# Optimization experiments

Measured on AMD Instinct MI355X. Metric: run time of the kernel, lower is better.

Reference implementation:

```python
import jax, jax.numpy as jnp
import numpy as np
import math

B, H, S, D = 2, 16, 2048, 64

def setup_inputs() -> dict:
    key = jax.random.key(0)
    kq, kk, kv, km = jax.random.split(key, 4)
    return {
        "query": jax.random.normal(kq, (B, H, S, D), dtype=jnp.float32),
        "key": jax.random.normal(kk, (B, H, S, D), dtype=jnp.float32),
        "value": jax.random.normal(kv, (B, H, S, D), dtype=jnp.float32),
        "attn_mask": jax.random.normal(km, (B, 1, S, S), dtype=jnp.float32),
    }

def reference(query, key, value, attn_mask):
    # qk = Q K^T / sqrt(D)  -> [B,H,S,S]
    scale = 1.0 / math.sqrt(query.shape[-1])
    qk = jnp.einsum("bhqd,bhkd->bhqk", query, key) * scale
    qk = qk + attn_mask  # additive mask, broadcasts over heads
    attn_weight = jax.nn.softmax(qk, axis=-1)
    # dropout_p = 0.0 (undefined global in source; p=0 train-mode dropout is identity)
    output = jnp.einsum("bhqk,bhkd->bhqd", attn_weight, value)
    return output
```

## Files before the change

### kernel.cpp

```cpp
#include <hip/hip_runtime.h>

#define B_ 2
#define H_ 16
#define S_ 2048
#define D_ 64

typedef __attribute__((ext_vector_type(8))) _Float16 half8;
typedef __attribute__((ext_vector_type(2))) __fp16 fp16x2;
typedef __attribute__((ext_vector_type(16))) float f32x16;

constexpr int QW  = 32;
constexpr int NW  = 2;
constexpr int QB  = QW * NW;
constexpr int KVB = 32;
constexpr int NIT = S_ / KVB;

__global__ __launch_bounds__(128, 2)
void fattn(const float* __restrict__ Qg, const float* __restrict__ Kg,
           const float* __restrict__ Vg, const float* __restrict__ Mg,
           float* __restrict__ Og)
{
    const int tid  = threadIdx.x;
    const int lo32 = tid & 31;
    const int hi   = (tid >> 5) & 1;
    const int wv   = tid >> 6;

    const int qblk = blockIdx.x;
    const int bh   = blockIdx.y;
    const int b    = bh >> 4;

    const float* Qp = Qg + (size_t)bh * S_ * D_;
    const float* Kp = Kg + (size_t)bh * S_ * D_;
    const float* Vp = Vg + (size_t)bh * S_ * D_;
    const float* Mp = Mg + (size_t)b  * S_ * S_;
    float*       Op = Og + (size_t)bh * S_ * D_;

    __shared__ __align__(16) _Float16 Khi[2][KVB * D_];
    __shared__ __align__(16) _Float16 Klo[2][KVB * D_];
    __shared__ __align__(16) _Float16 VThi[2][D_ * KVB];
    __shared__ __align__(16) _Float16 VTlo[2][D_ * KVB];

    const int qloc = qblk * QB + wv * QW + lo32;

    const int ksr = tid >> 2;
    const int ksc = tid & 3;
    const int vd  = tid & 63;
    const int vw  = tid >> 6;

    half8 Qhi[4], Qlo[4];
    #pragma unroll
    for (int f = 0; f < 4; ++f) {
        const float* src = Qp + (size_t)qloc * D_ + f * 16 + hi * 8;
        float4 a = *(const float4*)src;
        float4 c = *(const float4*)(src + 4);
        float v8[8] = {a.x, a.y, a.z, a.w, c.x, c.y, c.z, c.w};
        half8 hh, hl;
        #pragma unroll
        for (int j = 0; j < 8; ++j) {
            _Float16 h = (_Float16)v8[j];
            hh[j] = h;
            hl[j] = (_Float16)(v8[j] - (float)h);
        }
        Qhi[f] = hh; Qlo[f] = hl;
    }

    f32x16 acc0, acc1;
    #pragma unroll
    for (int i = 0; i < 16; ++i) { acc0[i] = 0.f; acc1[i] = 0.f; }
    float mrun = -1e30f, lrun = 0.f;

    const float kScL2 = 0.125f * 1.44269504088896340736f;
    const float kL2E  = 1.44269504088896340736f;

    float4 kr[4];
    float  vr[16];
    float4 mcur[4], mnxt[4];

    auto stage_load = [&](int kv) {
        const float* ks = Kp + (size_t)(kv + ksr) * D_ + ksc * 16;
        #pragma unroll
        for (int i = 0; i < 4; ++i) kr[i] = *(const float4*)(ks + 4 * i);
        const float* vs = Vp + (size_t)(kv + vw * 16) * D_ + vd;
        #pragma unroll
        for (int r = 0; r < 16; ++r) vr[r] = vs[(size_t)r * D_];
    };
    auto stage_write = [&](int bf) {
        #pragma unroll
        for (int u = 0; u < 2; ++u) {
            float e[8] = {kr[2*u].x, kr[2*u].y, kr[2*u].z, kr[2*u].w,
                          kr[2*u+1].x, kr[2*u+1].y, kr[2*u+1].z, kr[2*u+1].w};
            half8 hh, hl;
            #pragma unroll
            for (int j = 0; j < 8; ++j) {
                _Float16 h = (_Float16)e[j];
                hh[j] = h;
                hl[j] = (_Float16)(e[j] - (float)h);
            }
            const int cs = (ksc * 2 + u) ^ (ksr & 7);
            *(half8*)&Khi[bf][ksr * 64 + cs * 8] = hh;
            *(half8*)&Klo[bf][ksr * 64 + cs * 8] = hl;
        }
        #pragma unroll
        for (int u = 0; u < 2; ++u) {
            half8 hh, hl;
            #pragma unroll
            for (int j = 0; j < 8; ++j) {
                float x = vr[8*u + j];
                _Float16 h = (_Float16)x;
                hh[j] = h;
                hl[j] = (_Float16)(x - (float)h);
            }
            const int c = (vw * 2 + u) ^ (vd & 3) ^ ((vd >> 2) & 3);
            *(half8*)&VThi[bf][vd * 32 + c * 8] = hh;
            *(half8*)&VTlo[bf][vd * 32 + c * 8] = hl;
        }
    };
    auto mask_load = [&](int kv, float4* mv) {
        const float* mrow = Mp + (size_t)qloc * S_ + kv;
        #pragma unroll
        for (int g = 0; g < 4; ++g) mv[g] = *(const float4*)(mrow + 8 * g + 4 * hi);
    };

    stage_load(0);
    stage_write(0);
    mask_load(0, mcur);
    __syncthreads();

    for (int t = 0; t < NIT; ++t) {
        const int bf = t & 1;
        if (t + 1 < NIT) {
            mask_load((t + 1) * KVB, mnxt);
            stage_load((t + 1) * KVB);
        }

        f32x16 s;
        #pragma unroll
        for (int i = 0; i < 16; ++i) s[i] = 0.f;
        #pragma unroll
        for (int f = 0; f < 4; ++f) {
            const int cs = (2 * f + hi) ^ (lo32 & 7);
            half8 ah = *(const half8*)&Khi[bf][lo32 * 64 + cs * 8];
            half8 al = *(const half8*)&Klo[bf][lo32 * 64 + cs * 8];
            s = __builtin_amdgcn_mfma_f32_32x32x16_f16(ah, Qhi[f], s, 0, 0, 0);
            s = __builtin_amdgcn_mfma_f32_32x32x16_f16(al, Qhi[f], s, 0, 0, 0);
            s = __builtin_amdgcn_mfma_f32_32x32x16_f16(ah, Qlo[f], s, 0, 0, 0);
        }

        float p[16];
        #pragma unroll
        for (int g = 0; g < 4; ++g) {
            p[4*g+0] = fmaf(s[4*g+0], kScL2, mcur[g].x * kL2E);
            p[4*g+1] = fmaf(s[4*g+1], kScL2, mcur[g].y * kL2E);
            p[4*g+2] = fmaf(s[4*g+2], kScL2, mcur[g].z * kL2E);
            p[4*g+3] = fmaf(s[4*g+3], kScL2, mcur[g].w * kL2E);
        }

        float mt = p[0];
        #pragma unroll
        for (int r = 1; r < 16; ++r) mt = fmaxf(mt, p[r]);
        mt = fmaxf(mt, __shfl_xor(mt, 32));
        const float mnew = fmaxf(mrun, mt);
        const float corr = __builtin_amdgcn_exp2f(mrun - mnew);
        float ps = 0.f;
        #pragma unroll
        for (int r = 0; r < 16; ++r) {
            p[r] = __builtin_amdgcn_exp2f(p[r] - mnew);
            ps += p[r];
        }
        ps += __shfl_xor(ps, 32);
        lrun = lrun * corr + ps;
        mrun = mnew;
        #pragma unroll
        for (int i = 0; i < 16; ++i) { acc0[i] *= corr; acc1[i] *= corr; }

        int dw[8], px[8];
        #pragma unroll
        for (int g = 0; g < 4; ++g) {
            union { fp16x2 h; int i; } u0, u1;
            u0.h = __builtin_amdgcn_cvt_pkrtz(p[4*g+0], p[4*g+1]);
            u1.h = __builtin_amdgcn_cvt_pkrtz(p[4*g+2], p[4*g+3]);
            dw[2*g]   = u0.i;
            dw[2*g+1] = u1.i;
        }
        #pragma unroll
        for (int i = 0; i < 8; ++i) px[i] = __shfl_xor(dw[i], 32);

        half8 Pf[2];
        #pragma unroll
        for (int ks = 0; ks < 2; ++ks) {
            union { int i[4]; half8 h; } f;
            f.i[0] = hi ? px[4*ks+2] : dw[4*ks+0];
            f.i[1] = hi ? px[4*ks+3] : dw[4*ks+1];
            f.i[2] = hi ? dw[4*ks+2] : px[4*ks+0];
            f.i[3] = hi ? dw[4*ks+3] : px[4*ks+1];
            Pf[ks] = f.h;
        }

        #pragma unroll
        for (int ks = 0; ks < 2; ++ks) {
            const int c0 = (2 * ks + hi) ^ (lo32 & 3) ^ ((lo32 >> 2) & 3);
            half8 vh0 = *(const half8*)&VThi[bf][lo32        * 32 + c0 * 8];
            half8 vl0 = *(const half8*)&VTlo[bf][lo32        * 32 + c0 * 8];
            half8 vh1 = *(const half8*)&VThi[bf][(32 + lo32) * 32 + c0 * 8];
            half8 vl1 = *(const half8*)&VTlo[bf][(32 + lo32) * 32 + c0 * 8];
            acc0 = __builtin_amdgcn_mfma_f32_32x32x16_f16(vh0, Pf[ks], acc0, 0, 0, 0);
            acc0 = __builtin_amdgcn_mfma_f32_32x32x16_f16(vl0, Pf[ks], acc0, 0, 0, 0);
            acc1 = __builtin_amdgcn_mfma_f32_32x32x16_f16(vh1, Pf[ks], acc1, 0, 0, 0);
            acc1 = __builtin_amdgcn_mfma_f32_32x32x16_f16(vl1, Pf[ks], acc1, 0, 0, 0);
        }

        if (t + 1 < NIT) stage_write(bf ^ 1);
        #pragma unroll
        for (int g = 0; g < 4; ++g) mcur[g] = mnxt[g];
        __syncthreads();
    }

    const float inv = 1.0f / lrun;
    #pragma unroll
    for (int r = 0; r < 16; ++r) {
        const int drow = (r & 3) + 8 * (r >> 2) + 4 * hi;
        Op[(size_t)qloc * D_ + drow]      = acc0[r] * inv;
        Op[(size_t)qloc * D_ + 32 + drow] = acc1[r] * inv;
    }
}

extern "C" void kernel_launch(void* const* d_in, const int* in_sizes, int n_in,
                              void* d_out, int out_size, void* d_ws, size_t ws_size,
                              hipStream_t stream)
{
    (void)in_sizes; (void)n_in; (void)out_size; (void)d_ws; (void)ws_size;
    const float* Q = (const float*)d_in[0];
    const float* K = (const float*)d_in[1];
    const float* V = (const float*)d_in[2];
    const float* M = (const float*)d_in[3];
    float* O = (float*)d_out;

    dim3 grid(S_ / QB, B_ * H_);
    fattn<<<grid, 128, 0, stream>>>(Q, K, V, M, O);
}
```

Measured before the change: 241.0 us.

## Presplit K/V into fp16 hi/lo workspace and stream tiles via direct global-to-LDS loads

Adds a pre-pass kernel that converts K and V once into swizzled fp16 hi/lo tiles in the workspace. The attention kernel then copies each tile straight into LDS with global_load_lds, so each of the 32 query blocks per head no longer redoes the conversion and transpose work. It also adds a lazy rescale that skips the accumulator correction unless the running max grows by more than 8 (in log2 units). The cost is an extra kernel launch and a workspace round-trip, and it falls back to the old kernel if the workspace is too small.

```diff
diff --git a/kernel.cpp b/kernel.cpp
--- a/kernel.cpp
+++ b/kernel.cpp
@@ -14,6 +14,224 @@
 constexpr int QB  = QW * NW;
 constexpr int KVB = 32;
 constexpr int NIT = S_ / KVB;
+
+#define GLOBAL_AS(p) ((const __attribute__((address_space(1))) void*)(p))
+#define LDS_AS(p)    ((__attribute__((address_space(3))) void*)(p))
+
+__global__ __launch_bounds__(256)
+void presplit(const float* __restrict__ Kg, const float* __restrict__ Vg,
+              _Float16* __restrict__ W)
+{
+    const int t   = blockIdx.x;
+    const int bh  = blockIdx.y;
+    const int tid = threadIdx.x;
+
+    const float* Kp = Kg + (size_t)bh * S_ * D_ + (size_t)t * KVB * D_;
+    const float* Vp = Vg + (size_t)bh * S_ * D_ + (size_t)t * KVB * D_;
+    _Float16*    Wp = W + ((size_t)bh * NIT + t) * 8192;
+
+    {
+        const int r = tid >> 3, l = tid & 7;
+        const float* src = Kp + r * D_ + l * 8;
+        float4 a = *(const float4*)src;
+        float4 c = *(const float4*)(src + 4);
+        float e[8] = {a.x, a.y, a.z, a.w, c.x, c.y, c.z, c.w};
+        half8 hh, hl;
+        #pragma unroll
+        for (int j = 0; j < 8; ++j) {
+            _Float16 h = (_Float16)e[j];
+            hh[j] = h;
+            hl[j] = (_Float16)(e[j] - (float)h);
+        }
+        const int cs = l ^ (r & 7);
+        *(half8*)&Wp[r * 64 + cs * 8]        = hh;
+        *(half8*)&Wp[2048 + r * 64 + cs * 8] = hl;
+    }
+    {
+        const int d = tid & 63, c = tid >> 6;
+        float e[8];
+        #pragma unroll
+        for (int j = 0; j < 8; ++j) e[j] = Vp[(size_t)(c * 8 + j) * D_ + d];
+        half8 hh, hl;
+        #pragma unroll
+        for (int j = 0; j < 8; ++j) {
+            _Float16 h = (_Float16)e[j];
+            hh[j] = h;
+            hl[j] = (_Float16)(e[j] - (float)h);
+        }
+        const int cw = c ^ (d & 3) ^ ((d >> 2) & 3);
+        *(half8*)&Wp[4096 + d * 32 + cw * 8] = hh;
+        *(half8*)&Wp[6144 + d * 32 + cw * 8] = hl;
+    }
+}
+
+__global__ __launch_bounds__(128, 2)
+void fattn2(const float* __restrict__ Qg, const float* __restrict__ Mg,
+            const _Float16* __restrict__ W, float* __restrict__ Og)
+{
+    const int tid  = threadIdx.x;
+    const int lane = tid & 63;
+    const int lo32 = tid & 31;
+    const int hi   = (tid >> 5) & 1;
+    const int wv   = tid >> 6;
+
+    const int qblk = blockIdx.x;
+    const int bh   = blockIdx.y;
+    const int b    = bh >> 4;
+
+    const float* Qp = Qg + (size_t)bh * S_ * D_;
+    const float* Mp = Mg + (size_t)b  * S_ * S_;
+    float*       Op = Og + (size_t)bh * S_ * D_;
+    const _Float16* Wp = W + (size_t)bh * NIT * 8192;
+
+    __shared__ __align__(16) _Float16 TILE[2][8192];
+
+    const int qloc = qblk * QB + wv * QW + lo32;
+
+    half8 Qhi[4], Qlo[4];
+    #pragma unroll
+    for (int f = 0; f < 4; ++f) {
+        const float* src = Qp + (size_t)qloc * D_ + f * 16 + hi * 8;
+        float4 a = *(const float4*)src;
+        float4 c = *(const float4*)(src + 4);
+        float v8[8] = {a.x, a.y, a.z, a.w, c.x, c.y, c.z, c.w};
+        half8 hh, hl;
+        #pragma unroll
+        for (int j = 0; j < 8; ++j) {
+            _Float16 h = (_Float16)v8[j];
+            hh[j] = h;
+            hl[j] = (_Float16)(v8[j] - (float)h);
+        }
+        Qhi[f] = hh; Qlo[f] = hl;
+    }
+
+    f32x16 acc0, acc1;
+    #pragma unroll
+    for (int i = 0; i < 16; ++i) { acc0[i] = 0.f; acc1[i] = 0.f; }
+    float mrun = -1e30f, lrun = 0.f;
+
+    const float kScL2 = 0.125f * 1.44269504088896340736f;
+    const float kL2E  = 1.44269504088896340736f;
+
+    float4 mcur[4], mnxt[4];
+
+    auto stage = [&](int bf, int t) {
+        const _Float16* src = Wp + (size_t)t * 8192 + wv * 4096 + lane * 8;
+        _Float16* dst = &TILE[bf][wv * 4096];
+        #pragma unroll
+        for (int c = 0; c < 8; ++c)
+            __builtin_amdgcn_global_load_lds(GLOBAL_AS(src + c * 512),
+                                             LDS_AS(dst + c * 512), 16, 0, 0);
+    };
+    auto mask_load = [&](int kv, float4* mv) {
+        const float* mrow = Mp + (size_t)qloc * S_ + kv;
+        #pragma unroll
+        for (int g = 0; g < 4; ++g) mv[g] = *(const float4*)(mrow + 8 * g + 4 * hi);
+    };
+
+    stage(0, 0);
+    mask_load(0, mcur);
+    __syncthreads();
+
+    for (int t = 0; t < NIT; ++t) {
+        const int bf = t & 1;
+        if (t + 1 < NIT) {
+            mask_load((t + 1) * KVB, mnxt);
+            stage(bf ^ 1, t + 1);
+        }
+
+        f32x16 s;
+        #pragma unroll
+        for (int i = 0; i < 16; ++i) s[i] = 0.f;
+        #pragma unroll
+        for (int f = 0; f < 4; ++f) {
+            const int cs = (2 * f + hi) ^ (lo32 & 7);
+            half8 ah = *(const half8*)&TILE[bf][lo32 * 64 + cs * 8];
+            half8 al = *(const half8*)&TILE[bf][2048 + lo32 * 64 + cs * 8];
+            s = __builtin_amdgcn_mfma_f32_32x32x16_f16(ah, Qhi[f], s, 0, 0, 0);
+            s = __builtin_amdgcn_mfma_f32_32x32x16_f16(al, Qhi[f], s, 0, 0, 0);
+            s = __builtin_amdgcn_mfma_f32_32x32x16_f16(ah, Qlo[f], s, 0, 0, 0);
+        }
+
+        float p[16];
+        #pragma unroll
+        for (int g = 0; g < 4; ++g) {
+            p[4*g+0] = fmaf(s[4*g+0], kScL2, mcur[g].x * kL2E);
+            p[4*g+1] = fmaf(s[4*g+1], kScL2, mcur[g].y * kL2E);
+            p[4*g+2] = fmaf(s[4*g+2], kScL2, mcur[g].z * kL2E);
+            p[4*g+3] = fmaf(s[4*g+3], kScL2, mcur[g].w * kL2E);
+        }
+
+        float mt = p[0];
+        #pragma unroll
+        for (int r = 1; r < 16; ++r) mt = fmaxf(mt, p[r]);
+        mt = fmaxf(mt, __shfl_xor(mt, 32));
+        if (!__all(mt - mrun <= 8.0f)) {
+            const float mnew = fmaxf(mrun, mt);
+            const float corr = __builtin_amdgcn_exp2f(mrun - mnew);
+            lrun *= corr;
+            #pragma unroll
+            for (int i = 0; i < 16; ++i) { acc0[i] *= corr; acc1[i] *= corr; }
+            mrun = mnew;
+        }
+        float ps = 0.f;
+        #pragma unroll
+        for (int r = 0; r < 16; ++r) {
+            p[r] = __builtin_amdgcn_exp2f(p[r] - mrun);
+            ps += p[r];
+        }
+        ps += __shfl_xor(ps, 32);
+        lrun += ps;
+
+        int dw[8], px[8];
+        #pragma unroll
+        for (int g = 0; g < 4; ++g) {
+            union { fp16x2 h; int i; } u0, u1;
+            u0.h = __builtin_amdgcn_cvt_pkrtz(p[4*g+0], p[4*g+1]);
+            u1.h = __builtin_amdgcn_cvt_pkrtz(p[4*g+2], p[4*g+3]);
+            dw[2*g]   = u0.i;
+            dw[2*g+1] = u1.i;
+        }
+        #pragma unroll
+        for (int i = 0; i < 8; ++i) px[i] = __shfl_xor(dw[i], 32);
+
+        half8 Pf[2];
+        #pragma unroll
+        for (int ks = 0; ks < 2; ++ks) {
+            union { int i[4]; half8 h; } f;
+            f.i[0] = hi ? px[4*ks+2] : dw[4*ks+0];
+            f.i[1] = hi ? px[4*ks+3] : dw[4*ks+1];
+            f.i[2] = hi ? dw[4*ks+2] : px[4*ks+0];
+            f.i[3] = hi ? dw[4*ks+3] : px[4*ks+1];
+            Pf[ks] = f.h;
+        }
+
+        #pragma unroll
+        for (int ks = 0; ks < 2; ++ks) {
+            const int c0 = (2 * ks + hi) ^ (lo32 & 3) ^ ((lo32 >> 2) & 3);
+            half8 vh0 = *(const half8*)&TILE[bf][4096 + lo32        * 32 + c0 * 8];
+            half8 vl0 = *(const half8*)&TILE[bf][6144 + lo32        * 32 + c0 * 8];
+            half8 vh1 = *(const half8*)&TILE[bf][4096 + (32 + lo32) * 32 + c0 * 8];
+            half8 vl1 = *(const half8*)&TILE[bf][6144 + (32 + lo32) * 32 + c0 * 8];
+            acc0 = __builtin_amdgcn_mfma_f32_32x32x16_f16(vh0, Pf[ks], acc0, 0, 0, 0);
+            acc0 = __builtin_amdgcn_mfma_f32_32x32x16_f16(vl0, Pf[ks], acc0, 0, 0, 0);
+            acc1 = __builtin_amdgcn_mfma_f32_32x32x16_f16(vh1, Pf[ks], acc1, 0, 0, 0);
+            acc1 = __builtin_amdgcn_mfma_f32_32x32x16_f16(vl1, Pf[ks], acc1, 0, 0, 0);
+        }
+
+        #pragma unroll
+        for (int g = 0; g < 4; ++g) mcur[g] = mnxt[g];
+        __syncthreads();
+    }
+
+    const float inv = 1.0f / lrun;
+    #pragma unroll
+    for (int r = 0; r < 16; ++r) {
+        const int drow = (r & 3) + 8 * (r >> 2) + 4 * hi;
+        Op[(size_t)qloc * D_ + drow]      = acc0[r] * inv;
+        Op[(size_t)qloc * D_ + 32 + drow] = acc1[r] * inv;
+    }
+}
 
 __global__ __launch_bounds__(128, 2)
 void fattn(const float* __restrict__ Qg, const float* __restrict__ Kg,
@@ -228,13 +446,19 @@
                               void* d_out, int out_size, void* d_ws, size_t ws_size,
                               hipStream_t stream)
 {
-    (void)in_sizes; (void)n_in; (void)out_size; (void)d_ws; (void)ws_size;
+    (void)in_sizes; (void)n_in; (void)out_size;
     const float* Q = (const float*)d_in[0];
     const float* K = (const float*)d_in[1];
     const float* V = (const float*)d_in[2];
     const float* M = (const float*)d_in[3];
     float* O = (float*)d_out;
 
-    dim3 grid(S_ / QB, B_ * H_);
-    fattn<<<grid, 128, 0, stream>>>(Q, K, V, M, O);
+    const size_t need = (size_t)(B_ * H_) * NIT * 8192 * sizeof(_Float16);
+    if (ws_size >= need) {
+        _Float16* W = (_Float16*)d_ws;
+        presplit<<<dim3(NIT, B_ * H_), 256, 0, stream>>>(K, V, W);
+        fattn2<<<dim3(S_ / QB, B_ * H_), 128, 0, stream>>>(Q, M, W, O);
+    } else {
+        fattn<<<dim3(S_ / QB, B_ * H_), 128, 0, stream>>>(Q, K, V, M, O);
+    }
 }
```

Measured after the change: 230.0 us. 4.5% less time.
